# Kernel tuning notes

Hardware: AMD Instinct MI355X
Metric: run time of the kernel (lower is better)

Reference implementation:

```python
import jax, jax.numpy as jnp
import numpy as np

E = 1024
H = 16
F = 4096
EPS = 1e-5


def layer_norm(x, gamma, beta):
    mu = jnp.mean(x, axis=-1, keepdims=True)
    var = jnp.var(x, axis=-1, keepdims=True)
    return (x - mu) * jax.lax.rsqrt(var + EPS) * gamma + beta


def setup_inputs() -> dict:
    key = jax.random.key(0)
    ks = jax.random.split(key, 12)
    s = lambda d: 1.0 / np.sqrt(d)
    x = jax.random.normal(ks[0], (2, 2048, E), dtype=jnp.float32)
    Wq = jax.random.uniform(ks[1], (E, E), minval=-s(E), maxval=s(E))
    bq = jnp.zeros((E,), jnp.float32)
    Wk = jax.random.uniform(ks[2], (E, E), minval=-s(E), maxval=s(E))
    bk = jnp.zeros((E,), jnp.float32)
    Wv = jax.random.uniform(ks[3], (E, E), minval=-s(E), maxval=s(E))
    bv = jnp.zeros((E,), jnp.float32)
    Wo = jax.random.uniform(ks[4], (E, E), minval=-s(E), maxval=s(E))
    bo = jnp.zeros((E,), jnp.float32)
    g1 = jnp.ones((E,), jnp.float32)
    b1 = jnp.zeros((E,), jnp.float32)
    W1 = jax.random.uniform(ks[5], (E, F), minval=-s(E), maxval=s(E))
    bf1 = jnp.zeros((F,), jnp.float32)
    W2 = jax.random.uniform(ks[6], (F, E), minval=-s(F), maxval=s(F))
    bf2 = jnp.zeros((E,), jnp.float32)
    g2 = jnp.ones((E,), jnp.float32)
    b2 = jnp.zeros((E,), jnp.float32)
    return dict(x=x, Wq=Wq, bq=bq, Wk=Wk, bk=bk, Wv=Wv, bv=bv, Wo=Wo, bo=bo,
                g1=g1, b1=b1, W1=W1, bf1=bf1, W2=W2, bf2=bf2, g2=g2, b2=b2)


def reference(x, Wq, bq, Wk, bk, Wv, bv, Wo, bo, g1, b1, W1, bf1, W2, bf2, g2, b2):
    B, L, _ = x.shape
    Dh = E // H
    q = (x @ Wq + bq).reshape(B, L, H, Dh).transpose(0, 2, 1, 3)  # b h l d
    k = (x @ Wk + bk).reshape(B, L, H, Dh).transpose(0, 2, 1, 3)  # computed but unused (faithful to source)
    v = (x @ Wv + bv).reshape(B, L, H, Dh).transpose(0, 2, 1, 3)
    # NOTE: source computes scores as Q @ V^T (not K), scaled, then softmax
    scores = jnp.einsum('bhqd,bhkd->bhqk', q, v) / jnp.sqrt(jnp.float32(Dh))
    att = jax.nn.softmax(scores, axis=-1)
    ctx = jnp.einsum('bhqk,bhkd->bhqd', att, v)
    ctx = ctx.transpose(0, 2, 1, 3).reshape(B, L, E)
    att_out = ctx @ Wo + bo
    post_att = layer_norm(x + att_out, g1, b1)
    ff = jax.nn.relu(post_att @ W1 + bf1) @ W2 + bf2
    return layer_norm(post_att + ff, g2, b2)
```

## Files before the change

kernel.cpp:

```cpp
#include <hip/hip_runtime.h>
#include <stdint.h>

typedef unsigned short u16;
typedef __attribute__((ext_vector_type(8))) short short8;
typedef __attribute__((ext_vector_type(4))) float f32x4;
typedef __attribute__((ext_vector_type(4))) unsigned short u16x4;

#define TOKENS 4096
#define E_DIM 1024
#define F_DIM 4096
#define SEQ 2048
#define NH 16
#define DH 64

__device__ __forceinline__ u16 f2b(float f) {
  union { float f; unsigned u; } v; v.f = f;
  unsigned r = v.u + 0x7fffu + ((v.u >> 16) & 1u);
  return (u16)(r >> 16);
}

__device__ __forceinline__ void gl2lds16(const u16* g, u16* l) {
  __builtin_amdgcn_global_load_lds(
      (const __attribute__((address_space(1))) unsigned int*)(size_t)(g),
      (__attribute__((address_space(3))) unsigned int*)(unsigned int)(size_t)(l),
      16, 0, 0);
}


__global__ __launch_bounds__(256)
void transpose_w3(const float* __restrict__ W0, const float* __restrict__ W1s,
                  const float* __restrict__ W2s, u16* __restrict__ T0,
                  u16* __restrict__ T1, u16* __restrict__ T2) {
  __shared__ float tile[32][33];
  const float* W = (blockIdx.z == 0) ? W0 : (blockIdx.z == 1) ? W1s : W2s;
  u16* Wt = (blockIdx.z == 0) ? T0 : (blockIdx.z == 1) ? T1 : T2;
  const int kb = blockIdx.x * 32, nb = blockIdx.y * 32;
  const int tx = threadIdx.x & 31, ty = threadIdx.x >> 5;
#pragma unroll
  for (int i = 0; i < 32; i += 8)
    tile[ty + i][tx] = W[(size_t)(kb + ty + i) * 1024 + nb + tx];
  __syncthreads();
#pragma unroll
  for (int i = 0; i < 32; i += 8)
    Wt[(size_t)(nb + ty + i) * 1024 + kb + tx] = f2b(tile[tx][ty + i]);
}

__global__ __launch_bounds__(256)
void transpose_w(const float* __restrict__ W, u16* __restrict__ Wt, int K, int N) {
  __shared__ float tile[32][33];
  const int kb = blockIdx.x * 32, nb = blockIdx.y * 32;
  const int tx = threadIdx.x & 31, ty = threadIdx.x >> 5;
#pragma unroll
  for (int i = 0; i < 32; i += 8)
    tile[ty + i][tx] = W[(size_t)(kb + ty + i) * N + nb + tx];
  __syncthreads();
#pragma unroll
  for (int i = 0; i < 32; i += 8)
    Wt[(size_t)(nb + ty + i) * K + kb + tx] = f2b(tile[tx][ty + i]);
}

__global__ __launch_bounds__(256)
void f32_to_bf16(const float* __restrict__ in, u16* __restrict__ out) {
  const int i = blockIdx.x * 256 + threadIdx.x;
  f32x4 f = ((const f32x4*)in)[i];
  u16x4 u;
#pragma unroll
  for (int j = 0; j < 4; j++) u[j] = f2b(f[j]);
  ((u16x4*)out)[i] = u;
}

__global__ __launch_bounds__(256)
void transpose_v(const u16* __restrict__ vsrc, u16* __restrict__ vt) {
  __shared__ u16 tile[64][66];
  const int kb = blockIdx.x * 64;
  const int bh = blockIdx.y;
  const int b = bh >> 4, h = bh & 15;
  {
    const int d = threadIdx.x & 63, r = threadIdx.x >> 6;
#pragma unroll
    for (int i = 0; i < 64; i += 4)
      tile[r + i][d] = vsrc[(size_t)(b * SEQ + kb + r + i) * E_DIM + h * DH + d];
  }
  __syncthreads();
  {
    const int pos = threadIdx.x & 63;
    const int srck = (pos & 3) * 16 + (pos >> 2);
#pragma unroll
    for (int j = 0; j < 64; j += 4) {
      const int d = (threadIdx.x >> 6) + j;
      vt[(size_t)(bh * DH + d) * SEQ + kb + pos] = tile[srck][d];
    }
  }
}

template <int RELU, int OUTBF>
__global__ __launch_bounds__(512)
void gemm256(const u16* __restrict__ A, const u16* __restrict__ Bt,
             const float* __restrict__ bias, void* __restrict__ Cout,
             int N, int K) {
  __shared__ __align__(16) u16 lds[3][2][8192];
  const int tid = threadIdx.x;
  const int lane = tid & 63, wave = tid >> 6;
  const int wm = wave >> 2, wn = wave & 3;
  const int l15 = lane & 15, g = lane >> 4;

  const int bid = blockIdx.x;
  const int xcd = bid & 7, idx = bid >> 3;
  const int mT = (xcd >> 2) * 8 + (idx >> 2);
  const int nT = (xcd & 3) * 4 + (idx & 3);
  const int mBlk = mT * 256, nBlk = nT * 256;

  const u16* Ab = A + (size_t)mBlk * K;
  const u16* Bb = Bt + (size_t)nBlk * K;

  const int srow = lane >> 2;
  const int scolx = ((lane & 3) ^ ((lane >> 3) & 3)) * 8;
  const u16* sa0 = Ab + (size_t)(wave * 16 + srow) * K + scolx;
  const u16* sa1 = Ab + (size_t)((8 + wave) * 16 + srow) * K + scolx;
  const u16* sb0 = Bb + (size_t)(wave * 16 + srow) * K + scolx;
  const u16* sb1 = Bb + (size_t)((8 + wave) * 16 + srow) * K + scolx;

  const int fo = l15 * 32 + ((g ^ ((l15 >> 1) & 3)) << 3);

  f32x4 acc[8][4] = {};

  const int NT = K >> 5;

#define STAGE_A(buf, t)                                             \
  {                                                                 \
    gl2lds16(sa0 + (size_t)(t) * 32, &lds[buf][0][wave * 512 + lane * 8]);       \
    gl2lds16(sa1 + (size_t)(t) * 32, &lds[buf][0][(8 + wave) * 512 + lane * 8]); \
  }
#define STAGE_B(buf, t)                                             \
  {                                                                 \
    gl2lds16(sb0 + (size_t)(t) * 32, &lds[buf][1][wave * 512 + lane * 8]);       \
    gl2lds16(sb1 + (size_t)(t) * 32, &lds[buf][1][(8 + wave) * 512 + lane * 8]); \
  }

  STAGE_A(0, 0) STAGE_B(0, 0)
  STAGE_A(1, 1) STAGE_B(1, 1)
  asm volatile("s_waitcnt vmcnt(4)" ::: "memory");
  asm volatile("s_barrier" ::: "memory");

  int buf = 0, sbuf = 2;
  for (int t = 0; t < NT; ++t) {
    const u16* As_ = &lds[buf][0][wm * (8 * 512)];
    const u16* Bs_ = &lds[buf][1][wn * (4 * 512)];

    short8 af[4], bfr[4];
#pragma unroll
    for (int i = 0; i < 4; i++)
      af[i] = *(const short8*)(As_ + i * 512 + fo);
#pragma unroll
    for (int i = 0; i < 4; i++)
      bfr[i] = *(const short8*)(Bs_ + i * 512 + fo);
    if (t + 2 < NT) STAGE_A(sbuf, t + 2)
    asm volatile("s_barrier" ::: "memory");
    asm volatile("s_waitcnt lgkmcnt(0)" ::: "memory");
    __builtin_amdgcn_sched_barrier(0);
    __builtin_amdgcn_s_setprio(1);
#pragma unroll
    for (int mg = 0; mg < 4; mg++)
#pragma unroll
      for (int ng = 0; ng < 4; ng++)
        acc[mg][ng] = __builtin_amdgcn_mfma_f32_16x16x32_bf16(af[mg], bfr[ng],
                                                              acc[mg][ng], 0, 0, 0);
    __builtin_amdgcn_s_setprio(0);
    asm volatile("s_barrier" ::: "memory");

#pragma unroll
    for (int i = 0; i < 4; i++)
      af[i] = *(const short8*)(As_ + (4 + i) * 512 + fo);
    if (t + 2 < NT) STAGE_B(sbuf, t + 2)
    asm volatile("s_barrier" ::: "memory");
    asm volatile("s_waitcnt lgkmcnt(0)" ::: "memory");
    __builtin_amdgcn_sched_barrier(0);
    __builtin_amdgcn_s_setprio(1);
#pragma unroll
    for (int mg = 0; mg < 4; mg++)
#pragma unroll
      for (int ng = 0; ng < 4; ng++)
        acc[4 + mg][ng] = __builtin_amdgcn_mfma_f32_16x16x32_bf16(af[mg], bfr[ng],
                                                                  acc[4 + mg][ng], 0, 0, 0);
    __builtin_amdgcn_s_setprio(0);
    if (t + 2 < NT) asm volatile("s_waitcnt vmcnt(4)" ::: "memory");
    else            asm volatile("s_waitcnt vmcnt(0)" ::: "memory");
    asm volatile("s_barrier" ::: "memory");

    buf = (buf == 2) ? 0 : buf + 1;
    sbuf = (sbuf == 2) ? 0 : sbuf + 1;
  }
#undef STAGE_A
#undef STAGE_B

  const int row0 = mBlk + wm * 128 + g * 4;
  const int col0 = nBlk + wn * 64 + l15;
#pragma unroll
  for (int ng = 0; ng < 4; ng++) {
    const int c = col0 + ng * 16;
    const float bv = bias[c];
#pragma unroll
    for (int mg = 0; mg < 8; mg++) {
#pragma unroll
      for (int r = 0; r < 4; r++) {
        float v = acc[mg][ng][r] + bv;
        if (RELU) v = fmaxf(v, 0.f);
        const size_t o = (size_t)(row0 + mg * 16 + r) * N + c;
        if (OUTBF) ((u16*)Cout)[o] = f2b(v);
        else       ((float*)Cout)[o] = v;
      }
    }
  }
}

__global__ __launch_bounds__(512)
void gemm_wide_sk(const u16* __restrict__ A, const u16* __restrict__ Bt,
                  const float* __restrict__ bias, float* __restrict__ Cout,
                  int N, int K) {
  __shared__ __align__(16) u16 lds[3][12288];
  const int tid = threadIdx.x;
  const int lane = tid & 63, wave = tid >> 6;
  const int wm = wave >> 1, wn = wave & 1;
  const int l15 = lane & 15, g = lane >> 4;

  const int bid = blockIdx.x;
  const int xcd = bid & 7, idx = bid >> 3;
  const int kz = xcd & 1;
  const int nT = ((xcd >> 1) & 1) * 4 + (idx & 3);
  const int mT = (xcd >> 2) * 8 + (idx >> 2);
  const int mBlk = mT * 256, nBlk = nT * 128;
  const int Kh = K >> 1;

  const u16* Ab = A + (size_t)mBlk * K + (size_t)kz * Kh;
  const u16* Bb = Bt + (size_t)nBlk * K + (size_t)kz * Kh;

  const int srow = lane >> 2;
  const int scolx = ((lane & 3) ^ ((lane >> 3) & 3)) * 8;
  const u16* sa0 = Ab + (size_t)(wave * 16 + srow) * K + scolx;
  const u16* sa1 = Ab + (size_t)((8 + wave) * 16 + srow) * K + scolx;
  const u16* sb0 = Bb + (size_t)(wave * 16 + srow) * K + scolx;

  const int fo = l15 * 32 + ((g ^ ((l15 >> 1) & 3)) << 3);

  f32x4 acc[4][4] = {};
  const int NT = Kh >> 5;

#define WSTAGE(buf, t)                                                         \
  {                                                                            \
    gl2lds16(sa0 + (size_t)(t) * 32, &lds[buf][wave * 512 + lane * 8]);        \
    gl2lds16(sa1 + (size_t)(t) * 32, &lds[buf][(8 + wave) * 512 + lane * 8]);  \
    gl2lds16(sb0 + (size_t)(t) * 32, &lds[buf][8192 + wave * 512 + lane * 8]); \
  }

  WSTAGE(0, 0)
  WSTAGE(1, 1)
  asm volatile("s_waitcnt vmcnt(3)" ::: "memory");
  asm volatile("s_barrier" ::: "memory");

  int buf = 0, sbuf = 2;
  for (int t = 0; t < NT; ++t) {
    const u16* As_ = &lds[buf][wm * (4 * 512)];
    const u16* Bs_ = &lds[buf][8192 + wn * (4 * 512)];
    short8 af[4], bfr[4];
#pragma unroll
    for (int i = 0; i < 4; i++)
      af[i] = *(const short8*)(As_ + i * 512 + fo);
#pragma unroll
    for (int i = 0; i < 4; i++)
      bfr[i] = *(const short8*)(Bs_ + i * 512 + fo);
    if (t + 2 < NT) WSTAGE(sbuf, t + 2)
    asm volatile("s_waitcnt lgkmcnt(0)" ::: "memory");
    __builtin_amdgcn_sched_barrier(0);
    __builtin_amdgcn_s_setprio(1);
#pragma unroll
    for (int mi = 0; mi < 4; mi++)
#pragma unroll
      for (int ni = 0; ni < 4; ni++)
        acc[mi][ni] = __builtin_amdgcn_mfma_f32_16x16x32_bf16(af[mi], bfr[ni],
                                                              acc[mi][ni], 0, 0, 0);
    __builtin_amdgcn_s_setprio(0);
    if (t + 2 < NT) asm volatile("s_waitcnt vmcnt(3)" ::: "memory");
    else            asm volatile("s_waitcnt vmcnt(0)" ::: "memory");
    asm volatile("s_barrier" ::: "memory");
    buf = (buf == 2) ? 0 : buf + 1;
    sbuf = (sbuf == 2) ? 0 : sbuf + 1;
  }
#undef WSTAGE

  float* out = Cout + (size_t)kz * TOKENS * N;
  const int row0 = mBlk + wm * 64 + g * 4;
  const int col0 = nBlk + wn * 64 + l15;
#pragma unroll
  for (int ni = 0; ni < 4; ni++) {
    const int c = col0 + ni * 16;
    const float bv = (kz == 0) ? bias[c] : 0.f;
#pragma unroll
    for (int mi = 0; mi < 4; mi++) {
#pragma unroll
      for (int r = 0; r < 4; r++)
        out[(size_t)(row0 + mi * 16 + r) * N + c] = acc[mi][ni][r] + bv;
    }
  }
}

__global__ __launch_bounds__(512)
void gemm_qv(const u16* __restrict__ A, const u16* __restrict__ Bqv,
             const float* __restrict__ bq, const float* __restrict__ bv,
             u16* __restrict__ qout, u16* __restrict__ vout, int K) {
  __shared__ __align__(16) u16 lds[3][12288];
  const int tid = threadIdx.x;
  const int lane = tid & 63, wave = tid >> 6;
  const int wm = wave >> 1, wn = wave & 1;
  const int l15 = lane & 15, g = lane >> 4;

  const int bid = blockIdx.x;
  const int xcd = bid & 7, idx = bid >> 3;
  const int mT = (xcd >> 1) * 4 + (idx >> 3);
  const int nT = (xcd & 1) * 8 + (idx & 7);
  const int mBlk = mT * 256, nBlkG = nT * 128;

  const int isQ = nT < 8;
  const int ncol = isQ ? nBlkG : nBlkG - 1024;
  const float* bias = isQ ? bq : bv;
  u16* out = isQ ? qout : vout;
  const float oscale = isQ ? 0.125f * 1.44269504088896f : 1.0f;

  const u16* Ab = A + (size_t)mBlk * K;
  const u16* Bb = Bqv + (size_t)nBlkG * K;

  const int srow = lane >> 2;
  const int scolx = ((lane & 3) ^ ((lane >> 3) & 3)) * 8;
  const u16* sa0 = Ab + (size_t)(wave * 16 + srow) * K + scolx;
  const u16* sa1 = Ab + (size_t)((8 + wave) * 16 + srow) * K + scolx;
  const u16* sb0 = Bb + (size_t)(wave * 16 + srow) * K + scolx;

  const int fo = l15 * 32 + ((g ^ ((l15 >> 1) & 3)) << 3);

  f32x4 acc[4][4] = {};
  const int NT = K >> 5;

#define QSTAGE(buf, t)                                                         \
  {                                                                            \
    gl2lds16(sa0 + (size_t)(t) * 32, &lds[buf][wave * 512 + lane * 8]);        \
    gl2lds16(sa1 + (size_t)(t) * 32, &lds[buf][(8 + wave) * 512 + lane * 8]);  \
    gl2lds16(sb0 + (size_t)(t) * 32, &lds[buf][8192 + wave * 512 + lane * 8]); \
  }

  QSTAGE(0, 0)
  QSTAGE(1, 1)
  asm volatile("s_waitcnt vmcnt(3)" ::: "memory");
  asm volatile("s_barrier" ::: "memory");

  int buf = 0, sbuf = 2;
  for (int t = 0; t < NT; ++t) {
    const u16* As_ = &lds[buf][wm * (4 * 512)];
    const u16* Bs_ = &lds[buf][8192 + wn * (4 * 512)];
    short8 af[4], bfr[4];
#pragma unroll
    for (int i = 0; i < 4; i++)
      af[i] = *(const short8*)(As_ + i * 512 + fo);
#pragma unroll
    for (int i = 0; i < 4; i++)
      bfr[i] = *(const short8*)(Bs_ + i * 512 + fo);
    if (t + 2 < NT) QSTAGE(sbuf, t + 2)
    asm volatile("s_waitcnt lgkmcnt(0)" ::: "memory");
    __builtin_amdgcn_sched_barrier(0);
    __builtin_amdgcn_s_setprio(1);
#pragma unroll
    for (int mi = 0; mi < 4; mi++)
#pragma unroll
      for (int ni = 0; ni < 4; ni++)
        acc[mi][ni] = __builtin_amdgcn_mfma_f32_16x16x32_bf16(af[mi], bfr[ni],
                                                              acc[mi][ni], 0, 0, 0);
    __builtin_amdgcn_s_setprio(0);
    if (t + 2 < NT) asm volatile("s_waitcnt vmcnt(3)" ::: "memory");
    else            asm volatile("s_waitcnt vmcnt(0)" ::: "memory");
    asm volatile("s_barrier" ::: "memory");
    buf = (buf == 2) ? 0 : buf + 1;
    sbuf = (sbuf == 2) ? 0 : sbuf + 1;
  }
#undef QSTAGE

  const int row0 = mBlk + wm * 64 + g * 4;
  const int col0 = ncol + wn * 64 + l15;
#pragma unroll
  for (int ni = 0; ni < 4; ni++) {
    const int c = col0 + ni * 16;
    const float bv_ = bias[c];
#pragma unroll
    for (int mi = 0; mi < 4; mi++) {
#pragma unroll
      for (int r = 0; r < 4; r++) {
        float v = (acc[mi][ni][r] + bv_) * oscale;
        out[(size_t)(row0 + mi * 16 + r) * E_DIM + c] = f2b(v);
      }
    }
  }
}

__global__ __launch_bounds__(256)
void attn_kernel(const u16* __restrict__ qb, const u16* __restrict__ vb,
                 const u16* __restrict__ vtb, u16* __restrict__ ctxb) {
  __shared__ __align__(16) u16 Vs[2][4096];
  __shared__ __align__(16) u16 Vts[2][4096];
  __shared__ __align__(16) u16 Pl[4][1024];
  const int tid = threadIdx.x;
  const int lane = tid & 63;
  const int wave = tid >> 6;
  const int l15 = lane & 15;
  const int g = lane >> 4;
  const int l7 = l15 & 7;
  const int qblk = blockIdx.x;
  const int bh = blockIdx.y;
  const int b = bh >> 4;
  const int h = bh & 15;
  const int qrow = qblk * 64 + wave * 16;

  short8 aq0, aq1;
  {
    const u16* qp = qb + ((size_t)(b * SEQ + qrow + l15)) * E_DIM + h * DH + g * 8;
    aq0 = *(const short8*)(qp);
    aq1 = *(const short8*)(qp + 32);
  }

  f32x4 o[4] = {};
  float lsum[4] = {};

  u16* myPl = Pl[wave];

  const u16* qk0b0 = Vs[0] + l15 * 64 + ((g ^ l7) * 8);
  const u16* qk1b0 = Vs[0] + l15 * 64 + (((4 + g) ^ l7) * 8);
  const u16* bv0b0 = Vts[0] + l15 * 64 + ((g ^ l7) * 8);
  const u16* bv1b0 = Vts[0] + l15 * 64 + (((4 + g) ^ l7) * 8);
  const u16* ap0 = myPl + l15 * 64 + ((g ^ l7) << 3);
  const u16* ap1 = myPl + l15 * 64 + (((4 + g) ^ l7) << 3);
  u16* wr0 = myPl + (g * 4 + 0) * 64 + (((l15 >> 1) ^ ((g * 4 + 0) & 7)) << 3) + ((l15 & 1) << 2);
  u16* wr1 = myPl + (g * 4 + 1) * 64 + (((l15 >> 1) ^ ((g * 4 + 1) & 7)) << 3) + ((l15 & 1) << 2);
  u16* wr2 = myPl + (g * 4 + 2) * 64 + (((l15 >> 1) ^ ((g * 4 + 2) & 7)) << 3) + ((l15 & 1) << 2);
  u16* wr3 = myPl + (g * 4 + 3) * 64 + (((l15 >> 1) ^ ((g * 4 + 3) & 7)) << 3) + ((l15 & 1) << 2);

  const int srow = tid >> 3;
  const int sch = tid & 7;
  const int r0 = srow, r1 = 32 + srow;
  const u16* pv0 = vb + ((size_t)(b * SEQ) + r0) * E_DIM + h * DH + ((sch ^ (r0 & 7)) * 8);
  const u16* pv1 = vb + ((size_t)(b * SEQ) + r1) * E_DIM + h * DH + ((sch ^ (r1 & 7)) * 8);
  const u16* pt0 = vtb + ((size_t)bh * DH + r0) * SEQ + ((sch ^ (r0 & 7)) * 8);
  const u16* pt1 = vtb + ((size_t)bh * DH + r1) * SEQ + ((sch ^ (r1 & 7)) * 8);

#define STAGE(buf)                                      \
  {                                                     \
    gl2lds16(pv0, Vs[buf] + tid * 8);                   \
    gl2lds16(pv1, Vs[buf] + 2048 + tid * 8);            \
    gl2lds16(pt0, Vts[buf] + tid * 8);                  \
    gl2lds16(pt1, Vts[buf] + 2048 + tid * 8);           \
    pv0 += 64 * E_DIM; pv1 += 64 * E_DIM;               \
    pt0 += 64; pt1 += 64;                               \
  }

#define SMROW(r, WR)                                                          \
  {                                                                           \
    union { float f; unsigned u; } p0, p1, p2, p3;                            \
    p0.f = __builtin_amdgcn_exp2f(s[0][r]);                                   \
    p1.f = __builtin_amdgcn_exp2f(s[1][r]);                                   \
    p2.f = __builtin_amdgcn_exp2f(s[2][r]);                                   \
    p3.f = __builtin_amdgcn_exp2f(s[3][r]);                                   \
    union { unsigned u; float f; } t0, t1, t2, t3;                            \
    t0.u = p0.u & 0xffff0000u; t1.u = p1.u & 0xffff0000u;                     \
    t2.u = p2.u & 0xffff0000u; t3.u = p3.u & 0xffff0000u;                     \
    lsum[r] += (t0.f + t1.f) + (t2.f + t3.f);                                 \
    uint2 pk;                                                                 \
    pk.x = __builtin_amdgcn_perm(p1.u, p0.u, 0x07060302u);                    \
    pk.y = __builtin_amdgcn_perm(p3.u, p2.u, 0x07060302u);                    \
    *(uint2*)(WR) = pk;                                                       \
  }

#define COMPUTE(QK0, QK1, BV0, BV1)                                           \
  {                                                                           \
    f32x4 s[4];                                                               \
    _Pragma("unroll") for (int nt = 0; nt < 4; nt++) {                        \
      short8 b0 = *(const short8*)((QK0) + nt * 1024);                        \
      short8 b1 = *(const short8*)((QK1) + nt * 1024);                        \
      f32x4 z = {};                                                           \
      z = __builtin_amdgcn_mfma_f32_16x16x32_bf16(aq0, b0, z, 0, 0, 0);       \
      z = __builtin_amdgcn_mfma_f32_16x16x32_bf16(aq1, b1, z, 0, 0, 0);       \
      s[nt] = z;                                                              \
    }                                                                         \
    SMROW(0, wr0) SMROW(1, wr1) SMROW(2, wr2) SMROW(3, wr3)                   \
    {                                                                         \
      short8 ap = *(const short8*)ap0;                                        \
      _Pragma("unroll") for (int dt = 0; dt < 4; dt++) {                      \
        short8 bvv = *(const short8*)((BV0) + dt * 1024);                     \
        o[dt] = __builtin_amdgcn_mfma_f32_16x16x32_bf16(ap, bvv, o[dt], 0, 0, 0); \
      }                                                                       \
      ap = *(const short8*)ap1;                                               \
      _Pragma("unroll") for (int dt = 0; dt < 4; dt++) {                      \
        short8 bvv = *(const short8*)((BV1) + dt * 1024);                     \
        o[dt] = __builtin_amdgcn_mfma_f32_16x16x32_bf16(ap, bvv, o[dt], 0, 0, 0); \
      }                                                                       \
    }                                                                         \
  }

#define HALF(CB, EN)                                                          \
  {                                                                           \
    asm volatile("s_barrier" ::: "memory");                                   \
    if (EN) {                                                                 \
      STAGE(CB ^ 1)                                                           \
      asm volatile("s_waitcnt vmcnt(4)" ::: "memory");                        \
    } else {                                                                  \
      asm volatile("s_waitcnt vmcnt(0)" ::: "memory");                        \
    }                                                                         \
    asm volatile("s_barrier" ::: "memory");                                   \
    if (CB == 0) { COMPUTE(qk0b0, qk1b0, bv0b0, bv1b0) }                      \
    else { COMPUTE(qk0b0 + 4096, qk1b0 + 4096, bv0b0 + 4096, bv1b0 + 4096) }  \
  }

  STAGE(0)
#pragma unroll 1
  for (int it = 0; it < 15; ++it) {
    HALF(0, 1)
    HALF(1, 1)
  }
  HALF(0, 1)
  HALF(1, 0)

#undef HALF
#undef COMPUTE
#undef SMROW
#undef STAGE

#pragma unroll
  for (int r = 0; r < 4; r++) {
    float l = lsum[r];
    l += __shfl_xor(l, 1);
    l += __shfl_xor(l, 2);
    l += __shfl_xor(l, 4);
    l += __shfl_xor(l, 8);
    const float inv = 1.0f / l;
    size_t base = ((size_t)(b * SEQ + qrow + g * 4 + r)) * E_DIM + h * DH;
#pragma unroll
    for (int dt = 0; dt < 4; dt++)
      ctxb[base + dt * 16 + l15] = f2b(o[dt][r] * inv);
  }
}

__global__ __launch_bounds__(256)
void add_ln3(const float* __restrict__ X, const float* __restrict__ Y0,
             const float* __restrict__ Y1,
             const float* __restrict__ gam, const float* __restrict__ bet,
             float* __restrict__ out32, u16* __restrict__ out16) {
  const int row = blockIdx.x;
  const int tid = threadIdx.x;
  const size_t base = (size_t)row * E_DIM;
  const int c4 = tid * 4;
  f32x4 x = *(const f32x4*)(X + base + c4);
  f32x4 y0 = *(const f32x4*)(Y0 + base + c4);
  f32x4 y1 = *(const f32x4*)(Y1 + base + c4);
  f32x4 v;
  float s = 0.f, sq = 0.f;
#pragma unroll
  for (int i = 0; i < 4; i++) {
    float t = x[i] + y0[i] + y1[i];
    v[i] = t; s += t; sq += t * t;
  }
#pragma unroll
  for (int off = 32; off; off >>= 1) {
    s += __shfl_xor(s, off);
    sq += __shfl_xor(sq, off);
  }
  __shared__ float sh[8];
  const int wave = tid >> 6, lane = tid & 63;
  if (lane == 0) { sh[wave] = s; sh[4 + wave] = sq; }
  __syncthreads();
  s = sh[0] + sh[1] + sh[2] + sh[3];
  sq = sh[4] + sh[5] + sh[6] + sh[7];
  const float mean = s * (1.f / 1024.f);
  const float var = sq * (1.f / 1024.f) - mean * mean;
  const float rstd = rsqrtf(var + 1e-5f);
  f32x4 gm = *(const f32x4*)(gam + c4);
  f32x4 bt = *(const f32x4*)(bet + c4);
  f32x4 y;
  u16x4 yb;
#pragma unroll
  for (int i = 0; i < 4; i++) {
    y[i] = (v[i] - mean) * rstd * gm[i] + bt[i];
    yb[i] = f2b(y[i]);
  }
  *(f32x4*)(out32 + base + c4) = y;
  if (out16) *(u16x4*)(out16 + base + c4) = yb;
}

extern "C" void kernel_launch(void* const* d_in, const int* in_sizes, int n_in,
                              void* d_out, int out_size, void* d_ws, size_t ws_size,
                              hipStream_t stream) {
  const float* x   = (const float*)d_in[0];
  const float* Wq  = (const float*)d_in[1];
  const float* bq  = (const float*)d_in[2];
  const float* Wv  = (const float*)d_in[5];
  const float* bv  = (const float*)d_in[6];
  const float* Wo  = (const float*)d_in[7];
  const float* bo  = (const float*)d_in[8];
  const float* g1  = (const float*)d_in[9];
  const float* b1  = (const float*)d_in[10];
  const float* W1  = (const float*)d_in[11];
  const float* bf1 = (const float*)d_in[12];
  const float* W2  = (const float*)d_in[13];
  const float* bf2 = (const float*)d_in[14];
  const float* g2  = (const float*)d_in[15];
  const float* b2  = (const float*)d_in[16];

  char* w = (char*)d_ws;
  const size_t MB = 1024ull * 1024ull;
  u16*   xb   = (u16*)(w + 0);
  u16*   h1   = (u16*)(w + 8 * MB);
  u16*   qb   = (u16*)(w + 8 * MB);
  u16*   vb   = (u16*)(w + 16 * MB);
  u16*   vtb  = (u16*)(w + 24 * MB);
  u16*   ctxb = (u16*)(w + 32 * MB);
  float* att0 = (float*)(w + 40 * MB);
  float* ff0  = (float*)(w + 40 * MB);
  float* pa   = (float*)(w + 72 * MB);
  u16*   pab  = (u16*)(w + 88 * MB);
  u16*   WqT  = (u16*)(w + 96 * MB);
  u16*   WvT  = (u16*)(w + 98 * MB);
  u16*   WoT  = (u16*)(w + 100 * MB);
  u16*   W1T  = (u16*)(w + 102 * MB);
  u16*   W2T  = (u16*)(w + 110 * MB);

  transpose_w3<<<dim3(32, 32, 3), 256, 0, stream>>>(Wq, Wv, Wo, WqT, WvT, WoT);
  transpose_w<<<dim3(32, 128), 256, 0, stream>>>(W1, W1T, 1024, 4096);
  transpose_w<<<dim3(128, 32), 256, 0, stream>>>(W2, W2T, 4096, 1024);
  f32_to_bf16<<<TOKENS * E_DIM / 4 / 256, 256, 0, stream>>>(x, xb);

  gemm_qv<<<dim3(256), 512, 0, stream>>>(xb, WqT, bq, bv, qb, vb, 1024);
  transpose_v<<<dim3(32, 32), 256, 0, stream>>>(vb, vtb);
  attn_kernel<<<dim3(32, 32), 256, 0, stream>>>(qb, vb, vtb, ctxb);
  gemm_wide_sk<<<dim3(256), 512, 0, stream>>>(ctxb, WoT, bo, att0, 1024, 1024);
  add_ln3<<<TOKENS, 256, 0, stream>>>(x, att0, att0 + (size_t)TOKENS * 1024, g1, b1, pa, pab);
  gemm256<1, 1><<<dim3(256), 512, 0, stream>>>(pab, W1T, bf1, h1, 4096, 1024);
  gemm_wide_sk<<<dim3(256), 512, 0, stream>>>(h1, W2T, bf2, ff0, 1024, 4096);
  add_ln3<<<TOKENS, 256, 0, stream>>>(pa, ff0, ff0 + (size_t)TOKENS * 1024, g2, b2, (float*)d_out, (u16*)nullptr);
}
```

Before: 343.2 us.

## Keep attention probabilities in registers by swapping MFMA operands for QK^T

The score MFMA now takes the key tile as the A operand, producing S^T, so each lane holds probabilities for one query row across key positions. Those values can be packed straight into the A-fragment of the P·V MFMA without going through LDS. The V transpose kernel permutes key order to match the new fragment layout. This removes the per-wave LDS scratch for P, its writes and reads, and the associated waits. Row sums now reduce across lane groups with a final shuffle, and correctness depends on the permutation matching the fragment mapping exactly.

After: 341.2 us. Within noise of the previous version (-0.6%).

```diff
diff --git a/kernel.cpp b/kernel.cpp
--- a/kernel.cpp
+++ b/kernel.cpp
@@ -84,7 +84,8 @@
   __syncthreads();
   {
     const int pos = threadIdx.x & 63;
-    const int srck = (pos & 3) * 16 + (pos >> 2);
+    const int srck = ((pos >> 5) << 5) | (((pos >> 2) & 1) << 4) |
+                     (((pos >> 3) & 3) << 2) | (pos & 3);
 #pragma unroll
     for (int j = 0; j < 64; j += 4) {
       const int d = (threadIdx.x >> 6) + j;
@@ -403,7 +404,6 @@
                  const u16* __restrict__ vtb, u16* __restrict__ ctxb) {
   __shared__ __align__(16) u16 Vs[2][4096];
   __shared__ __align__(16) u16 Vts[2][4096];
-  __shared__ __align__(16) u16 Pl[4][1024];
   const int tid = threadIdx.x;
   const int lane = tid & 63;
   const int wave = tid >> 6;
@@ -424,20 +424,12 @@
   }
 
   f32x4 o[4] = {};
-  float lsum[4] = {};
-
-  u16* myPl = Pl[wave];
+  float lsum = 0.f;
 
   const u16* qk0b0 = Vs[0] + l15 * 64 + ((g ^ l7) * 8);
   const u16* qk1b0 = Vs[0] + l15 * 64 + (((4 + g) ^ l7) * 8);
   const u16* bv0b0 = Vts[0] + l15 * 64 + ((g ^ l7) * 8);
   const u16* bv1b0 = Vts[0] + l15 * 64 + (((4 + g) ^ l7) * 8);
-  const u16* ap0 = myPl + l15 * 64 + ((g ^ l7) << 3);
-  const u16* ap1 = myPl + l15 * 64 + (((4 + g) ^ l7) << 3);
-  u16* wr0 = myPl + (g * 4 + 0) * 64 + (((l15 >> 1) ^ ((g * 4 + 0) & 7)) << 3) + ((l15 & 1) << 2);
-  u16* wr1 = myPl + (g * 4 + 1) * 64 + (((l15 >> 1) ^ ((g * 4 + 1) & 7)) << 3) + ((l15 & 1) << 2);
-  u16* wr2 = myPl + (g * 4 + 2) * 64 + (((l15 >> 1) ^ ((g * 4 + 2) & 7)) << 3) + ((l15 & 1) << 2);
-  u16* wr3 = myPl + (g * 4 + 3) * 64 + (((l15 >> 1) ^ ((g * 4 + 3) & 7)) << 3) + ((l15 & 1) << 2);
 
   const int srow = tid >> 3;
   const int sch = tid & 7;
@@ -457,23 +449,6 @@
     pt0 += 64; pt1 += 64;                               \
   }
 
-#define SMROW(r, WR)                                                          \
-  {                                                                           \
-    union { float f; unsigned u; } p0, p1, p2, p3;                            \
-    p0.f = __builtin_amdgcn_exp2f(s[0][r]);                                   \
-    p1.f = __builtin_amdgcn_exp2f(s[1][r]);                                   \
-    p2.f = __builtin_amdgcn_exp2f(s[2][r]);                                   \
-    p3.f = __builtin_amdgcn_exp2f(s[3][r]);                                   \
-    union { unsigned u; float f; } t0, t1, t2, t3;                            \
-    t0.u = p0.u & 0xffff0000u; t1.u = p1.u & 0xffff0000u;                     \
-    t2.u = p2.u & 0xffff0000u; t3.u = p3.u & 0xffff0000u;                     \
-    lsum[r] += (t0.f + t1.f) + (t2.f + t3.f);                                 \
-    uint2 pk;                                                                 \
-    pk.x = __builtin_amdgcn_perm(p1.u, p0.u, 0x07060302u);                    \
-    pk.y = __builtin_amdgcn_perm(p3.u, p2.u, 0x07060302u);                    \
-    *(uint2*)(WR) = pk;                                                       \
-  }
-
 #define COMPUTE(QK0, QK1, BV0, BV1)                                           \
   {                                                                           \
     f32x4 s[4];                                                               \
@@ -481,22 +456,40 @@
       short8 b0 = *(const short8*)((QK0) + nt * 1024);                        \
       short8 b1 = *(const short8*)((QK1) + nt * 1024);                        \
       f32x4 z = {};                                                           \
-      z = __builtin_amdgcn_mfma_f32_16x16x32_bf16(aq0, b0, z, 0, 0, 0);       \
-      z = __builtin_amdgcn_mfma_f32_16x16x32_bf16(aq1, b1, z, 0, 0, 0);       \
+      z = __builtin_amdgcn_mfma_f32_16x16x32_bf16(b0, aq0, z, 0, 0, 0);       \
+      z = __builtin_amdgcn_mfma_f32_16x16x32_bf16(b1, aq1, z, 0, 0, 0);       \
       s[nt] = z;                                                              \
     }                                                                         \
-    SMROW(0, wr0) SMROW(1, wr1) SMROW(2, wr2) SMROW(3, wr3)                   \
+    union { unsigned w[4]; short8 v; } pa0, pa1;                              \
     {                                                                         \
-      short8 ap = *(const short8*)ap0;                                        \
-      _Pragma("unroll") for (int dt = 0; dt < 4; dt++) {                      \
-        short8 bvv = *(const short8*)((BV0) + dt * 1024);                     \
-        o[dt] = __builtin_amdgcn_mfma_f32_16x16x32_bf16(ap, bvv, o[dt], 0, 0, 0); \
+      unsigned pu[4][4];                                                      \
+      float ls = 0.f;                                                         \
+      _Pragma("unroll") for (int nt = 0; nt < 4; nt++) {                      \
+        _Pragma("unroll") for (int r = 0; r < 4; r++) {                       \
+          union { float f; unsigned u; } e;                                   \
+          e.f = __builtin_amdgcn_exp2f(s[nt][r]);                             \
+          pu[nt][r] = e.u;                                                    \
+          union { unsigned u; float f; } t; t.u = e.u & 0xffff0000u;          \
+          ls += t.f;                                                          \
+        }                                                                     \
       }                                                                       \
-      ap = *(const short8*)ap1;                                               \
-      _Pragma("unroll") for (int dt = 0; dt < 4; dt++) {                      \
-        short8 bvv = *(const short8*)((BV1) + dt * 1024);                     \
-        o[dt] = __builtin_amdgcn_mfma_f32_16x16x32_bf16(ap, bvv, o[dt], 0, 0, 0); \
-      }                                                                       \
+      lsum += ls;                                                             \
+      pa0.w[0] = __builtin_amdgcn_perm(pu[0][1], pu[0][0], 0x07060302u);      \
+      pa0.w[1] = __builtin_amdgcn_perm(pu[0][3], pu[0][2], 0x07060302u);      \
+      pa0.w[2] = __builtin_amdgcn_perm(pu[1][1], pu[1][0], 0x07060302u);      \
+      pa0.w[3] = __builtin_amdgcn_perm(pu[1][3], pu[1][2], 0x07060302u);      \
+      pa1.w[0] = __builtin_amdgcn_perm(pu[2][1], pu[2][0], 0x07060302u);      \
+      pa1.w[1] = __builtin_amdgcn_perm(pu[2][3], pu[2][2], 0x07060302u);      \
+      pa1.w[2] = __builtin_amdgcn_perm(pu[3][1], pu[3][0], 0x07060302u);      \
+      pa1.w[3] = __builtin_amdgcn_perm(pu[3][3], pu[3][2], 0x07060302u);      \
+    }                                                                         \
+    _Pragma("unroll") for (int dt = 0; dt < 4; dt++) {                        \
+      short8 bvv = *(const short8*)((BV0) + dt * 1024);                       \
+      o[dt] = __builtin_amdgcn_mfma_f32_16x16x32_bf16(pa0.v, bvv, o[dt], 0, 0, 0); \
+    }                                                                         \
+    _Pragma("unroll") for (int dt = 0; dt < 4; dt++) {                        \
+      short8 bvv = *(const short8*)((BV1) + dt * 1024);                       \
+      o[dt] = __builtin_amdgcn_mfma_f32_16x16x32_bf16(pa1.v, bvv, o[dt], 0, 0, 0); \
     }                                                                         \
   }
 
@@ -525,17 +518,13 @@
 
 #undef HALF
 #undef COMPUTE
-#undef SMROW
 #undef STAGE
 
+  lsum += __shfl_xor(lsum, 16);
+  lsum += __shfl_xor(lsum, 32);
 #pragma unroll
   for (int r = 0; r < 4; r++) {
-    float l = lsum[r];
-    l += __shfl_xor(l, 1);
-    l += __shfl_xor(l, 2);
-    l += __shfl_xor(l, 4);
-    l += __shfl_xor(l, 8);
-    const float inv = 1.0f / l;
+    const float inv = 1.0f / __shfl(lsum, g * 4 + r);
     size_t base = ((size_t)(b * SEQ + qrow + g * 4 + r)) * E_DIM + h * DH;
 #pragma unroll
     for (int dt = 0; dt < 4; dt++)
```
